# Performance work log

Measured on AMD Instinct MI355X. Metric: run time of the kernel, lower is better.

## Reference

```python
import jax, jax.numpy as jnp
import numpy as np

N = 10000
E = 160000
IN_C = 512
OUT_C = 1024
NEG_SLOPE = 0.2


def setup_inputs() -> dict:
    key = jax.random.key(0)
    ks = jax.random.split(key, 12)
    x = jax.random.normal(ks[0], (N, IN_C), dtype=jnp.float32)
    edge_index = jax.random.randint(ks[1], (2, E), 0, N, dtype=jnp.int32)
    s_in = 1.0 / np.sqrt(IN_C)
    s_out = 1.0 / np.sqrt(OUT_C)
    return {
        "x": x,
        "edge_index": edge_index,
        "W1": jax.random.normal(ks[2], (IN_C, OUT_C), dtype=jnp.float32) * s_in,
        "a_src1": jax.random.normal(ks[3], (OUT_C,), dtype=jnp.float32) * s_out,
        "a_dst1": jax.random.normal(ks[4], (OUT_C,), dtype=jnp.float32) * s_out,
        "b1": jnp.zeros((OUT_C,), dtype=jnp.float32),
        "W2": jax.random.normal(ks[5], (IN_C, OUT_C), dtype=jnp.float32) * s_in,
        "a_src2": jax.random.normal(ks[6], (OUT_C,), dtype=jnp.float32) * s_out,
        "a_dst2": jax.random.normal(ks[7], (OUT_C,), dtype=jnp.float32) * s_out,
        "b2": jnp.zeros((OUT_C,), dtype=jnp.float32),
        "prelu_a": jnp.asarray(0.25, dtype=jnp.float32),
        "Wp1": jax.random.normal(ks[8], (OUT_C, OUT_C), dtype=jnp.float32) * s_out,
        "bp1": jnp.zeros((OUT_C,), dtype=jnp.float32),
        "Wp2": jax.random.normal(ks[9], (OUT_C, 1024), dtype=jnp.float32) * s_out,
    }


def _gat_conv(x, src, dst, W, a_src, a_dst, b):
    # x: [N, in], W: [in, out]. PyG GATConv, heads=1, self-loops already in src/dst.
    h = x @ W  # [N, out]
    alpha_s = h @ a_src  # [N]
    alpha_d = h @ a_dst  # [N]
    e = alpha_s[src] + alpha_d[dst]  # [E+N]
    e = jnp.where(e >= 0, e, NEG_SLOPE * e)  # LeakyReLU(0.2)
    # segment softmax over destination nodes
    m = jax.ops.segment_max(e, dst, num_segments=N)  # [N]
    ex = jnp.exp(e - m[dst])
    denom = jax.ops.segment_sum(ex, dst, num_segments=N)  # [N], >=1 via self-loops
    alpha = ex / denom[dst]  # [E+N]
    out = jax.ops.segment_sum(alpha[:, None] * h[src], dst, num_segments=N)
    return out + b


def reference(x, edge_index, W1, a_src1, a_dst1, b1, W2, a_src2, a_dst2, b2,
              prelu_a, Wp1, bp1, Wp2):
    # add self loops (PyG GATConv default)
    loops = jnp.arange(N, dtype=edge_index.dtype)
    src = jnp.concatenate([edge_index[0], loops])
    dst = jnp.concatenate([edge_index[1], loops])

    def prelu(v):
        return jnp.where(v >= 0, v, prelu_a * v)

    h1 = prelu(_gat_conv(x, src, dst, W1, a_src1, a_dst1, b1))  # [N, 1024]
    h2 = prelu(_gat_conv(x, src, dst, W2, a_src2, a_dst2, b2))  # [N, 1024]
    h = h1 + h2

    # semantic attention: project -> mean over nodes -> softmax over 1024 dims
    w = jnp.tanh(h @ Wp1 + bp1) @ Wp2  # [N, 1024]
    w = w.mean(axis=0)  # [1024]
    att = jax.nn.softmax(w, axis=0)  # [1024] == beta.mean(0).squeeze()
    return att * h1 + (1.0 - att) * h2
```

## Files before the change

kernel.cpp:

```cpp
#include <hip/hip_runtime.h>

#define IN_C 512
#define OUT_C 1024
#define NC2 2048
#define NEG_SLOPE 0.2f

typedef short frag8 __attribute__((ext_vector_type(8)));
typedef float f32x4 __attribute__((ext_vector_type(4)));

#define GLOAD_LDS16(g, l) __builtin_amdgcn_global_load_lds(\
    (const __attribute__((address_space(1))) void*)(g), \
    (__attribute__((address_space(3))) void*)(l), 16, 0, 0)

__device__ __forceinline__ unsigned short f2b(float f){
  unsigned u = __float_as_uint(f);
  unsigned r = (u + 0x7fffu + ((u >> 16) & 1u)) >> 16;
  return (unsigned short)r;
}
__device__ __forceinline__ float leaky(float v){ return v >= 0.f ? v : NEG_SLOPE * v; }


__global__ void prep_kernel(const float* __restrict__ W1, const float* __restrict__ W2,
                            const float* __restrict__ Wp1,
                            const float* __restrict__ a_src1, const float* __restrict__ a_dst1,
                            const float* __restrict__ a_src2, const float* __restrict__ a_dst2,
                            unsigned short* __restrict__ WT, unsigned short* __restrict__ Wp1T,
                            float* __restrict__ uv){
  __shared__ float tile[32][33];
  int b = blockIdx.x;
  int tx = threadIdx.x & 31, ty = threadIdx.x >> 5;
  if (b < 1024){
    const float* in = (b >> 9) ? W2 : W1;
    int rowOff = (b >> 9) * OUT_C;
    int bb = b & 511;
    int c0 = (bb & 31) * 32, r0 = (bb >> 5) * 32;
    for (int i = ty; i < 32; i += 8)
      tile[i][tx] = in[(size_t)(r0 + i) * OUT_C + c0 + tx];
    __syncthreads();
    for (int i = ty; i < 32; i += 8)
      WT[(size_t)(c0 + i + rowOff) * IN_C + r0 + tx] = f2b(tile[tx][i]);
  } else if (b < 2048){
    int bb = b - 1024;
    int c0 = (bb & 31) * 32, r0 = (bb >> 5) * 32;
    for (int i = ty; i < 32; i += 8)
      tile[i][tx] = Wp1[(size_t)(r0 + i) * OUT_C + c0 + tx];
    __syncthreads();
    for (int i = ty; i < 32; i += 8)
      Wp1T[(size_t)(c0 + i) * OUT_C + r0 + tx] = f2b(tile[tx][i]);
  } else {
    int g = (b - 2048) * 4 + (threadIdx.x >> 6);
    int lane = threadIdx.x & 63;
    int which = g >> 9;
    int i = g & 511;
    const float* W = (which < 2) ? W1 : W2;
    const float* a = (which == 0) ? a_src1 : (which == 1) ? a_dst1 : (which == 2) ? a_src2 : a_dst2;
    const float* row = W + (size_t)i * OUT_C;
    float s = 0.f;
    for (int j = lane; j < OUT_C; j += 64) s += row[j] * a[j];
    for (int off = 32; off; off >>= 1) s += __shfl_down(s, off);
    if (lane == 0) uv[which * IN_C + i] = s;
  }
}


__global__ void alpha_kernel(const float* __restrict__ x, const float* __restrict__ uv,
                             unsigned short* __restrict__ xb,
                             float* __restrict__ as1, float* __restrict__ ad1,
                             float* __restrict__ as2, float* __restrict__ ad2,
                             float* __restrict__ self1, float* __restrict__ self2,
                             int* counts, int* cursor, float* colsum, float* wv){
  int n = blockIdx.x;
  int w = threadIdx.x >> 6, lane = threadIdx.x & 63;
  __shared__ float sh[4];
  if (threadIdx.x == 0){ counts[n] = 0; cursor[n] = 0; }
  if (n < 8){
    int i = n * 256 + threadIdx.x;
    if (i < 1024) colsum[i] = 0.f; else wv[i - 1024] = 0.f;
  }
  const float4* rv = (const float4*)(x + (size_t)n * IN_C);
  const float4* un = (const float4*)(uv + w * IN_C);
  float4 v0 = rv[lane], v1 = rv[lane + 64];
  float4 u0 = un[lane], u1 = un[lane + 64];
  float s = v0.x*u0.x + v0.y*u0.y + v0.z*u0.z + v0.w*u0.w
          + v1.x*u1.x + v1.y*u1.y + v1.z*u1.z + v1.w*u1.w;
  if (w == 0){
    ushort4 p0, p1;
    p0.x = f2b(v0.x); p0.y = f2b(v0.y); p0.z = f2b(v0.z); p0.w = f2b(v0.w);
    p1.x = f2b(v1.x); p1.y = f2b(v1.y); p1.z = f2b(v1.z); p1.w = f2b(v1.w);
    *(ushort4*)(xb + (size_t)n * IN_C + lane * 4) = p0;
    *(ushort4*)(xb + (size_t)n * IN_C + 256 + lane * 4) = p1;
  }
  for (int off = 32; off; off >>= 1) s += __shfl_down(s, off);
  if (lane == 0){
    sh[w] = s;
    if (w == 0) as1[n] = s;
    else if (w == 1) ad1[n] = s;
    else if (w == 2) as2[n] = s;
    else ad2[n] = s;
  }
  __syncthreads();
  if (threadIdx.x == 0){
    self1[n] = leaky(sh[0] + sh[1]);
    self2[n] = leaky(sh[2] + sh[3]);
  }
}


__global__ void histcount_kernel(const int* __restrict__ dst, int* counts, int E){
  int e = blockIdx.x * 256 + threadIdx.x;
  if (e < E) atomicAdd(&counts[dst[e]], 1);
}

__global__ void scanA_kernel(const int* __restrict__ counts, int* __restrict__ offs,
                             int* __restrict__ bsum, int n){
  __shared__ int wsum[4];
  int i = blockIdx.x * 256 + threadIdx.x;
  int wave = threadIdx.x >> 6, lane = threadIdx.x & 63;
  int v = (i < n) ? counts[i] : 0;
  int sc = v;
  for (int o = 1; o < 64; o <<= 1){
    int t = __shfl_up(sc, o);
    if (lane >= o) sc += t;
  }
  if (lane == 63) wsum[wave] = sc;
  __syncthreads();
  int wp = 0, tot = 0;
#pragma unroll
  for (int k = 0; k < 4; k++){
    int ws = wsum[k];
    if (k < wave) wp += ws;
    tot += ws;
  }
  if (i < n) offs[i] = wp + sc - v;
  if (threadIdx.x == 0) bsum[blockIdx.x] = tot;
}

__global__ void scanB_kernel(int* __restrict__ bsum, int nb){
  int lane = threadIdx.x;
  int v = (lane < nb) ? bsum[lane] : 0;
  int sc = v;
  for (int o = 1; o < 64; o <<= 1){
    int t = __shfl_up(sc, o);
    if (lane >= o) sc += t;
  }
  if (lane < nb) bsum[lane] = sc - v;
}

__global__ void scanC_kernel(int* __restrict__ offs, const int* __restrict__ bsum,
                             const float* __restrict__ self1, const float* __restrict__ self2,
                             float* __restrict__ den1, float* __restrict__ den2, int n){
  int i = blockIdx.x * 256 + threadIdx.x;
  if (i >= n) return;
  offs[i] += bsum[blockIdx.x];
  den1[i] = expf(self1[i]);
  den2[i] = expf(self2[i]);
}

__global__ void scatterexp_kernel(const int* __restrict__ src, const int* __restrict__ dst,
                                  const int* __restrict__ offs, int* cursor,
                                  const float* __restrict__ as1, const float* __restrict__ ad1,
                                  const float* __restrict__ as2, const float* __restrict__ ad2,
                                  int* __restrict__ nsrc, float* __restrict__ nw1, float* __restrict__ nw2,
                                  float* den1, float* den2, int E){
  int e = blockIdx.x * 256 + threadIdx.x;
  if (e >= E) return;
  int s = src[e], d = dst[e];
  int p = atomicAdd(&cursor[d], 1);
  int idx = offs[d] + p;
  float x1 = expf(leaky(as1[s] + ad1[d]));
  float x2 = expf(leaky(as2[s] + ad2[d]));
  nsrc[idx] = s; nw1[idx] = x1; nw2[idx] = x2;
  atomicAdd(&den1[d], x1);
  atomicAdd(&den2[d], x2);
}


#define AGG_FMA8(ACC, W, U) \
  ACC[0] += (W) * __uint_as_float(((unsigned)(U).x) << 16); \
  ACC[1] += (W) * __uint_as_float(((unsigned)(U).x) & 0xffff0000u); \
  ACC[2] += (W) * __uint_as_float(((unsigned)(U).y) << 16); \
  ACC[3] += (W) * __uint_as_float(((unsigned)(U).y) & 0xffff0000u); \
  ACC[4] += (W) * __uint_as_float(((unsigned)(U).z) << 16); \
  ACC[5] += (W) * __uint_as_float(((unsigned)(U).z) & 0xffff0000u); \
  ACC[6] += (W) * __uint_as_float(((unsigned)(U).w) << 16); \
  ACC[7] += (W) * __uint_as_float(((unsigned)(U).w) & 0xffff0000u);

__global__ __launch_bounds__(256) void aggx_kernel(
    const int* __restrict__ counts, const int* __restrict__ offs,
    const int* __restrict__ nsrc, const float* __restrict__ nw1, const float* __restrict__ nw2,
    const float* __restrict__ den1, const float* __restrict__ den2,
    const float* __restrict__ self1, const float* __restrict__ self2,
    const unsigned short* __restrict__ xb,
    unsigned short* __restrict__ xa1b, unsigned short* __restrict__ xa2b, int N){
  int wid = threadIdx.x >> 6, lane = threadIdx.x & 63;
  int d = blockIdx.x * 4 + wid;
  if (d >= N) return;
  float inv1 = 1.f / den1[d], inv2 = 1.f / den2[d];
  int deg = counts[d], off = offs[d];
  float acc1[8] = {0,0,0,0,0,0,0,0}, acc2[8] = {0,0,0,0,0,0,0,0};
  const unsigned short* Xb = xb + lane * 8;
  for (int base = 0; base < deg; base += 64){
    int i = base + lane;
    int s = 0; float w1 = 0.f, w2 = 0.f;
    if (i < deg){
      int p = off + i;
      s = nsrc[p];
      w1 = nw1[p] * inv1;
      w2 = nw2[p] * inv2;
    }
    int cnt = min(64, deg - base);
#pragma unroll 4
    for (int j = 0; j < cnt; j++){
      int sj = __shfl(s, j);
      float w1j = __shfl(w1, j);
      float w2j = __shfl(w2, j);
      int4 u = *(const int4*)(Xb + (size_t)sj * IN_C);
      AGG_FMA8(acc1, w1j, u)
      AGG_FMA8(acc2, w2j, u)
    }
  }
  {
    float ws1 = expf(self1[d]) * inv1;
    float ws2 = expf(self2[d]) * inv2;
    int4 u = *(const int4*)(Xb + (size_t)d * IN_C);
    AGG_FMA8(acc1, ws1, u)
    AGG_FMA8(acc2, ws2, u)
  }
  size_t outb = (size_t)d * IN_C + lane * 8;
  int4 o1, o2;
  o1.x = (int)((unsigned)f2b(acc1[0]) | ((unsigned)f2b(acc1[1]) << 16));
  o1.y = (int)((unsigned)f2b(acc1[2]) | ((unsigned)f2b(acc1[3]) << 16));
  o1.z = (int)((unsigned)f2b(acc1[4]) | ((unsigned)f2b(acc1[5]) << 16));
  o1.w = (int)((unsigned)f2b(acc1[6]) | ((unsigned)f2b(acc1[7]) << 16));
  o2.x = (int)((unsigned)f2b(acc2[0]) | ((unsigned)f2b(acc2[1]) << 16));
  o2.y = (int)((unsigned)f2b(acc2[2]) | ((unsigned)f2b(acc2[3]) << 16));
  o2.z = (int)((unsigned)f2b(acc2[4]) | ((unsigned)f2b(acc2[5]) << 16));
  o2.w = (int)((unsigned)f2b(acc2[6]) | ((unsigned)f2b(acc2[7]) << 16));
  *(int4*)(xa1b + outb) = o1;
  *(int4*)(xa2b + outb) = o2;
}


__global__ __launch_bounds__(256) void gemmh_kernel(const unsigned short* __restrict__ A1,
                                                    const unsigned short* __restrict__ A2,
                                                    const unsigned short* __restrict__ BT,
                                                    const float* __restrict__ b1,
                                                    const float* __restrict__ b2,
                                                    const float* __restrict__ prelu_a,
                                                    unsigned short* __restrict__ hsum,
                                                    unsigned short* __restrict__ hdiff,
                                                    int M, int Mtiles, int perx){
  const int bid = blockIdx.x;
  const int xcd = bid & 7;
  const int li = bid >> 3;
  const int bn_t = li & 7;
  const int bm_t = xcd * perx + (li >> 3);
  if (bm_t >= Mtiles) return;
  const int bm = bm_t * 64, bn = bn_t * 128;
  __shared__ unsigned short Al[64 * 32];
  __shared__ unsigned short Bl[128 * 32];
  const int t = threadIdx.x;
  const int lane = t & 63, wid = t >> 6;
  const int wj = wid;
  const int l16 = lane & 15, q = lane >> 4;
  const int lch = (lane & 3) * 8;
  f32x4 acc1[4][2] = {};
  f32x4 acc2[4][2] = {};
  const int arow = bm + wid * 16 + (lane >> 2);
  const int brow0 = bn + wid * 32 + (lane >> 2);
  const int ga = min(arow, M - 1);
  const unsigned short* pa1 = A1 + (size_t)ga * IN_C + lch;
  const unsigned short* pa2 = A2 + (size_t)ga * IN_C + lch;
  const unsigned short* pb0 = BT + (size_t)brow0 * IN_C + lch;
  const unsigned short* pb1 = BT + (size_t)(brow0 + 16) * IN_C + lch;
  const size_t boff2 = (size_t)OUT_C * IN_C;
  for (int k0 = 0; k0 < IN_C; k0 += 32){
    GLOAD_LDS16(pa1 + k0, &Al[(wid * 16) * 32]);
    GLOAD_LDS16(pb0 + k0, &Bl[(wid * 32) * 32]);
    GLOAD_LDS16(pb1 + k0, &Bl[(wid * 32 + 16) * 32]);
    __syncthreads();
    frag8 af[4], bf[2];
#pragma unroll
    for (int mi = 0; mi < 4; mi++) af[mi] = *(const frag8*)&Al[(mi*16 + l16) * 32 + q*8];
#pragma unroll
    for (int nj = 0; nj < 2; nj++) bf[nj] = *(const frag8*)&Bl[(wj*32 + nj*16 + l16) * 32 + q*8];
#pragma unroll
    for (int mi = 0; mi < 4; mi++)
#pragma unroll
      for (int nj = 0; nj < 2; nj++)
        acc1[mi][nj] = __builtin_amdgcn_mfma_f32_16x16x32_bf16(af[mi], bf[nj], acc1[mi][nj], 0, 0, 0);
    __syncthreads();
  }
  for (int k0 = 0; k0 < IN_C; k0 += 32){
    GLOAD_LDS16(pa2 + k0, &Al[(wid * 16) * 32]);
    GLOAD_LDS16(pb0 + boff2 + k0, &Bl[(wid * 32) * 32]);
    GLOAD_LDS16(pb1 + boff2 + k0, &Bl[(wid * 32 + 16) * 32]);
    __syncthreads();
    frag8 af[4], bf[2];
#pragma unroll
    for (int mi = 0; mi < 4; mi++) af[mi] = *(const frag8*)&Al[(mi*16 + l16) * 32 + q*8];
#pragma unroll
    for (int nj = 0; nj < 2; nj++) bf[nj] = *(const frag8*)&Bl[(wj*32 + nj*16 + l16) * 32 + q*8];
#pragma unroll
    for (int mi = 0; mi < 4; mi++)
#pragma unroll
      for (int nj = 0; nj < 2; nj++)
        acc2[mi][nj] = __builtin_amdgcn_mfma_f32_16x16x32_bf16(af[mi], bf[nj], acc2[mi][nj], 0, 0, 0);
    __syncthreads();
  }
  float pa = prelu_a[0];
#pragma unroll
  for (int mi = 0; mi < 4; mi++){
#pragma unroll
    for (int r = 0; r < 4; r++){
      int row = bm + mi*16 + q*4 + r;
      if (row >= M) continue;
#pragma unroll
      for (int nj = 0; nj < 2; nj++){
        int col = bn + wj*32 + nj*16 + l16;
        float v1 = acc1[mi][nj][r] + b1[col];
        v1 = v1 >= 0.f ? v1 : pa * v1;
        float v2 = acc2[mi][nj][r] + b2[col];
        v2 = v2 >= 0.f ? v2 : pa * v2;
        size_t idx = (size_t)row * OUT_C + col;
        hsum[idx]  = f2b(v1 + v2);
        hdiff[idx] = f2b(v1 - v2);
      }
    }
  }
}


__global__ __launch_bounds__(256) void gemm2_kernel(const unsigned short* __restrict__ A,
                                                    const unsigned short* __restrict__ BT,
                                                    const float* __restrict__ bp1,
                                                    float* __restrict__ colsum,
                                                    int M, int Mtiles, int perx){
  const int bid = blockIdx.x;
  const int xcd = bid & 7;
  const int li = bid >> 3;
  const int bn_t = li & 7;
  const int bm_t = xcd * perx + (li >> 3);
  if (bm_t >= Mtiles) return;
  const int bm = bm_t * 64, bn = bn_t * 128;
  __shared__ unsigned short Al[64 * 32];
  __shared__ unsigned short Bl[128 * 32];
  __shared__ float cs[128];
  const int t = threadIdx.x;
  const int lane = t & 63, wid = t >> 6;
  const int wj = wid;
  const int l16 = lane & 15, q = lane >> 4;
  const int lch = (lane & 3) * 8;
  if (t < 128) cs[t] = 0.f;
  f32x4 acc[4][2] = {};
  const int arow = bm + wid * 16 + (lane >> 2);
  const int brow0 = bn + wid * 32 + (lane >> 2);
  const int ga = min(arow, M - 1);
  const unsigned short* pa = A + (size_t)ga * OUT_C + lch;
  const unsigned short* pb0 = BT + (size_t)brow0 * OUT_C + lch;
  const unsigned short* pb1 = BT + (size_t)(brow0 + 16) * OUT_C + lch;
  for (int k0 = 0; k0 < OUT_C; k0 += 32){
    GLOAD_LDS16(pa + k0, &Al[(wid * 16) * 32]);
    GLOAD_LDS16(pb0 + k0, &Bl[(wid * 32) * 32]);
    GLOAD_LDS16(pb1 + k0, &Bl[(wid * 32 + 16) * 32]);
    __syncthreads();
    frag8 af[4], bf[2];
#pragma unroll
    for (int mi = 0; mi < 4; mi++) af[mi] = *(const frag8*)&Al[(mi*16 + l16) * 32 + q*8];
#pragma unroll
    for (int nj = 0; nj < 2; nj++) bf[nj] = *(const frag8*)&Bl[(wj*32 + nj*16 + l16) * 32 + q*8];
#pragma unroll
    for (int mi = 0; mi < 4; mi++)
#pragma unroll
      for (int nj = 0; nj < 2; nj++)
        acc[mi][nj] = __builtin_amdgcn_mfma_f32_16x16x32_bf16(af[mi], bf[nj], acc[mi][nj], 0, 0, 0);
    __syncthreads();
  }
#pragma unroll
  for (int nj = 0; nj < 2; nj++){
    int col = bn + wj*32 + nj*16 + l16;
    float bias = bp1[col];
    float p = 0.f;
#pragma unroll
    for (int mi = 0; mi < 4; mi++){
#pragma unroll
      for (int r = 0; r < 4; r++){
        int row = bm + mi*16 + q*4 + r;
        float tv = tanhf(acc[mi][nj][r] + bias);
        if (row < M) p += tv;
      }
    }
    p += __shfl_xor(p, 16);
    p += __shfl_xor(p, 32);
    if (q == 0) atomicAdd(&cs[wj*32 + nj*16 + l16], p);
  }
  __syncthreads();
  if (t < 128) atomicAdd(&colsum[bn + t], cs[t]);
}


__global__ void wproj_kernel(const float* __restrict__ colsum, const float* __restrict__ Wp2,
                             float* __restrict__ wv){
  int o = blockIdx.x * 256 + threadIdx.x;
  int c0 = blockIdx.y * 128;
  float acc = 0.f;
  for (int c = c0; c < c0 + 128; c++) acc += colsum[c] * Wp2[(size_t)c * OUT_C + o];
  atomicAdd(&wv[o], acc);
}

__global__ __launch_bounds__(1024) void softmax_kernel(const float* __restrict__ wv,
                                                       float* __restrict__ att, float invN){
  int o = threadIdx.x;
  __shared__ float red[1024];
  float w = wv[o] * invN;
  red[o] = w; __syncthreads();
  for (int s = 512; s > 0; s >>= 1){ if (o < s) red[o] = fmaxf(red[o], red[o + s]); __syncthreads(); }
  float m = red[0]; __syncthreads();
  float e = expf(w - m);
  red[o] = e; __syncthreads();
  for (int s = 512; s > 0; s >>= 1){ if (o < s) red[o] += red[o + s]; __syncthreads(); }
  att[o] = e / red[0];
}

__global__ void combine_kernel(const float* __restrict__ att, const unsigned short* __restrict__ hs,
                               const unsigned short* __restrict__ hd, float* __restrict__ out, int total8){
  int i = blockIdx.x * 256 + threadIdx.x;
  if (i >= total8) return;
  int colb = (i & 127) * 8;
  int4 us = ((const int4*)hs)[i];
  int4 ud = ((const int4*)hd)[i];
  float4 a0 = *(const float4*)(att + colb);
  float4 a1 = *(const float4*)(att + colb + 4);
  float o[8]; float sv, dv;
  sv = __uint_as_float(((unsigned)us.x) << 16);        dv = __uint_as_float(((unsigned)ud.x) << 16);
  o[0] = 0.5f * sv + (a0.x - 0.5f) * dv;
  sv = __uint_as_float(((unsigned)us.x) & 0xffff0000u); dv = __uint_as_float(((unsigned)ud.x) & 0xffff0000u);
  o[1] = 0.5f * sv + (a0.y - 0.5f) * dv;
  sv = __uint_as_float(((unsigned)us.y) << 16);        dv = __uint_as_float(((unsigned)ud.y) << 16);
  o[2] = 0.5f * sv + (a0.z - 0.5f) * dv;
  sv = __uint_as_float(((unsigned)us.y) & 0xffff0000u); dv = __uint_as_float(((unsigned)ud.y) & 0xffff0000u);
  o[3] = 0.5f * sv + (a0.w - 0.5f) * dv;
  sv = __uint_as_float(((unsigned)us.z) << 16);        dv = __uint_as_float(((unsigned)ud.z) << 16);
  o[4] = 0.5f * sv + (a1.x - 0.5f) * dv;
  sv = __uint_as_float(((unsigned)us.z) & 0xffff0000u); dv = __uint_as_float(((unsigned)ud.z) & 0xffff0000u);
  o[5] = 0.5f * sv + (a1.y - 0.5f) * dv;
  sv = __uint_as_float(((unsigned)us.w) << 16);        dv = __uint_as_float(((unsigned)ud.w) << 16);
  o[6] = 0.5f * sv + (a1.z - 0.5f) * dv;
  sv = __uint_as_float(((unsigned)us.w) & 0xffff0000u); dv = __uint_as_float(((unsigned)ud.w) & 0xffff0000u);
  o[7] = 0.5f * sv + (a1.w - 0.5f) * dv;
  float4 f0; f0.x = o[0]; f0.y = o[1]; f0.z = o[2]; f0.w = o[3];
  float4 f1; f1.x = o[4]; f1.y = o[5]; f1.z = o[6]; f1.w = o[7];
  *(float4*)(out + (size_t)i * 8) = f0;
  *(float4*)(out + (size_t)i * 8 + 4) = f1;
}


extern "C" void kernel_launch(void* const* d_in, const int* in_sizes, int n_in,
                              void* d_out, int out_size, void* d_ws, size_t ws_size,
                              hipStream_t stream){
  const float* x      = (const float*)d_in[0];
  const int*   edge   = (const int*)d_in[1];
  const float* W1     = (const float*)d_in[2];
  const float* a_src1 = (const float*)d_in[3];
  const float* a_dst1 = (const float*)d_in[4];
  const float* b1     = (const float*)d_in[5];
  const float* W2     = (const float*)d_in[6];
  const float* a_src2 = (const float*)d_in[7];
  const float* a_dst2 = (const float*)d_in[8];
  const float* b2     = (const float*)d_in[9];
  const float* prelu_a= (const float*)d_in[10];
  const float* Wp1    = (const float*)d_in[11];
  const float* bp1    = (const float*)d_in[12];
  const float* Wp2    = (const float*)d_in[13];
  const int N = in_sizes[0] / IN_C;
  const int E = in_sizes[1] / 2;
  const int* srcArr = edge;
  const int* dstArr = edge + E;

  char* ws = (char*)d_ws;
  size_t o = 0;
  auto alloc = [&](size_t b) -> char* {
    char* p = ws + o;
    o = (o + b + 255) & ~(size_t)255;
    return p;
  };
  unsigned short* xb    = (unsigned short*)alloc((size_t)N * IN_C * 2);
  unsigned short* WT    = (unsigned short*)alloc((size_t)NC2 * IN_C * 2);
  unsigned short* Wp1T  = (unsigned short*)alloc((size_t)OUT_C * OUT_C * 2);
  unsigned short* xa1b  = (unsigned short*)alloc((size_t)N * IN_C * 2);
  unsigned short* xa2b  = (unsigned short*)alloc((size_t)N * IN_C * 2);
  unsigned short* hsum  = (unsigned short*)alloc((size_t)N * OUT_C * 2);
  unsigned short* hdiff = (unsigned short*)alloc((size_t)N * OUT_C * 2);
  float*          uv    = (float*)alloc(4 * IN_C * 4);
  float*          as1   = (float*)alloc((size_t)4 * N * 4);
  float* ad1 = as1 + N; float* as2 = as1 + 2 * N; float* ad2 = as1 + 3 * N;
  float*          self1 = (float*)alloc((size_t)2 * N * 4); float* self2 = self1 + N;
  float*          den1  = (float*)alloc((size_t)2 * N * 4); float* den2 = den1 + N;
  int*            counts= (int*)alloc((size_t)N * 4);
  int*            offs  = (int*)alloc((size_t)(N + 1) * 4);
  int*            cursor= (int*)alloc((size_t)N * 4);
  int*            bsum  = (int*)alloc(64 * 4);
  int*            nsrc  = (int*)alloc((size_t)E * 4);
  float*          nw1   = (float*)alloc((size_t)E * 4);
  float*          nw2   = (float*)alloc((size_t)E * 4);
  float*          colsum= (float*)alloc(OUT_C * 4);
  float*          wv    = (float*)alloc(OUT_C * 4);
  float*          att   = (float*)alloc(OUT_C * 4);

  const int Mtiles = (N + 63) / 64;
  const int perx = (Mtiles + 7) / 8;
  const int gemmgrid = 8 * perx * 8;
  const int nchunk = (N + 255) / 256;

  prep_kernel<<<2560, 256, 0, stream>>>(W1, W2, Wp1, a_src1, a_dst1, a_src2, a_dst2, WT, Wp1T, uv);
  alpha_kernel<<<N, 256, 0, stream>>>(x, uv, xb, as1, ad1, as2, ad2, self1, self2,
                                      counts, cursor, colsum, wv);
  histcount_kernel<<<(E + 255) / 256, 256, 0, stream>>>(dstArr, counts, E);
  scanA_kernel<<<nchunk, 256, 0, stream>>>(counts, offs, bsum, N);
  scanB_kernel<<<1, 64, 0, stream>>>(bsum, nchunk);
  scanC_kernel<<<nchunk, 256, 0, stream>>>(offs, bsum, self1, self2, den1, den2, N);
  scatterexp_kernel<<<(E + 255) / 256, 256, 0, stream>>>(srcArr, dstArr, offs, cursor,
                                                         as1, ad1, as2, ad2,
                                                         nsrc, nw1, nw2, den1, den2, E);
  aggx_kernel<<<(N + 3) / 4, 256, 0, stream>>>(counts, offs, nsrc, nw1, nw2, den1, den2,
                                               self1, self2, xb, xa1b, xa2b, N);
  gemmh_kernel<<<gemmgrid, 256, 0, stream>>>(xa1b, xa2b, WT, b1, b2, prelu_a,
                                             hsum, hdiff, N, Mtiles, perx);
  gemm2_kernel<<<gemmgrid, 256, 0, stream>>>(hsum, Wp1T, bp1, colsum, N, Mtiles, perx);
  wproj_kernel<<<dim3(4, 8), 256, 0, stream>>>(colsum, Wp2, wv);
  softmax_kernel<<<1, 1024, 0, stream>>>(wv, att, 1.0f / (float)N);
  combine_kernel<<<(N * OUT_C / 8 + 255) / 256, 256, 0, stream>>>(att, hsum, hdiff, (float*)d_out,
                                                                  N * OUT_C / 8);
}
```

Before: 295.3 us.

## Fuse graph preprocessing kernels and compute softmax weights inside aggregation

```diff
diff --git a/kernel.cpp b/kernel.cpp
--- a/kernel.cpp
+++ b/kernel.cpp
@@ -25,7 +25,8 @@
                             const float* __restrict__ a_src1, const float* __restrict__ a_dst1,
                             const float* __restrict__ a_src2, const float* __restrict__ a_dst2,
                             unsigned short* __restrict__ WT, unsigned short* __restrict__ Wp1T,
-                            float* __restrict__ uv){
+                            float* __restrict__ uv, int* __restrict__ counts,
+                            int* __restrict__ cursor, int N){
   __shared__ float tile[32][33];
   int b = blockIdx.x;
   int tx = threadIdx.x & 31, ty = threadIdx.x >> 5;
@@ -47,7 +48,7 @@
     __syncthreads();
     for (int i = ty; i < 32; i += 8)
       Wp1T[(size_t)(c0 + i) * OUT_C + r0 + tx] = f2b(tile[tx][i]);
-  } else {
+  } else if (b < 2560){
     int g = (b - 2048) * 4 + (threadIdx.x >> 6);
     int lane = threadIdx.x & 63;
     int which = g >> 9;
@@ -59,20 +60,30 @@
     for (int j = lane; j < OUT_C; j += 64) s += row[j] * a[j];
     for (int off = 32; off; off >>= 1) s += __shfl_down(s, off);
     if (lane == 0) uv[which * IN_C + i] = s;
-  }
-}
-
-
-__global__ void alpha_kernel(const float* __restrict__ x, const float* __restrict__ uv,
-                             unsigned short* __restrict__ xb,
-                             float* __restrict__ as1, float* __restrict__ ad1,
-                             float* __restrict__ as2, float* __restrict__ ad2,
-                             float* __restrict__ self1, float* __restrict__ self2,
-                             int* counts, int* cursor, float* colsum, float* wv){
-  int n = blockIdx.x;
+  } else {
+    int i = (b - 2560) * 256 + threadIdx.x;
+    if (i < N){ counts[i] = 0; cursor[i] = 0; }
+  }
+}
+
+
+__global__ void alphahist_kernel(const float* __restrict__ x, const float* __restrict__ uv,
+                                 const int* __restrict__ dst,
+                                 unsigned short* __restrict__ xb,
+                                 float2* __restrict__ sa, float2* __restrict__ da,
+                                 float2* __restrict__ ese,
+                                 int* __restrict__ counts,
+                                 float* __restrict__ colsum, float* __restrict__ wv,
+                                 int N, int E){
+  int b = blockIdx.x;
+  if (b >= N){
+    int e = (b - N) * 256 + threadIdx.x;
+    if (e < E) atomicAdd(&counts[dst[e]], 1);
+    return;
+  }
+  int n = b;
   int w = threadIdx.x >> 6, lane = threadIdx.x & 63;
   __shared__ float sh[4];
-  if (threadIdx.x == 0){ counts[n] = 0; cursor[n] = 0; }
   if (n < 8){
     int i = n * 256 + threadIdx.x;
     if (i < 1024) colsum[i] = 0.f; else wv[i - 1024] = 0.f;
@@ -91,87 +102,56 @@
     *(ushort4*)(xb + (size_t)n * IN_C + 256 + lane * 4) = p1;
   }
   for (int off = 32; off; off >>= 1) s += __shfl_down(s, off);
-  if (lane == 0){
-    sh[w] = s;
-    if (w == 0) as1[n] = s;
-    else if (w == 1) ad1[n] = s;
-    else if (w == 2) as2[n] = s;
-    else ad2[n] = s;
-  }
+  if (lane == 0) sh[w] = s;
   __syncthreads();
   if (threadIdx.x == 0){
-    self1[n] = leaky(sh[0] + sh[1]);
-    self2[n] = leaky(sh[2] + sh[3]);
-  }
-}
-
-
-__global__ void histcount_kernel(const int* __restrict__ dst, int* counts, int E){
-  int e = blockIdx.x * 256 + threadIdx.x;
-  if (e < E) atomicAdd(&counts[dst[e]], 1);
-}
-
-__global__ void scanA_kernel(const int* __restrict__ counts, int* __restrict__ offs,
-                             int* __restrict__ bsum, int n){
-  __shared__ int wsum[4];
-  int i = blockIdx.x * 256 + threadIdx.x;
-  int wave = threadIdx.x >> 6, lane = threadIdx.x & 63;
-  int v = (i < n) ? counts[i] : 0;
-  int sc = v;
-  for (int o = 1; o < 64; o <<= 1){
-    int t = __shfl_up(sc, o);
-    if (lane >= o) sc += t;
-  }
-  if (lane == 63) wsum[wave] = sc;
+    float2 vsa; vsa.x = sh[0]; vsa.y = sh[2];
+    float2 vda; vda.x = sh[1]; vda.y = sh[3];
+    sa[n] = vsa; da[n] = vda;
+    float2 es;
+    es.x = expf(leaky(sh[0] + sh[1]));
+    es.y = expf(leaky(sh[2] + sh[3]));
+    ese[n] = es;
+  }
+}
+
+
+__global__ __launch_bounds__(1024) void scan_kernel(const int* __restrict__ counts,
+                                                    int* __restrict__ offs, int n){
+  __shared__ int ws[16];
+  __shared__ int base_s;
+  int tid = threadIdx.x, lane = tid & 63, wave = tid >> 6;
+  if (tid == 0) base_s = 0;
   __syncthreads();
-  int wp = 0, tot = 0;
-#pragma unroll
-  for (int k = 0; k < 4; k++){
-    int ws = wsum[k];
-    if (k < wave) wp += ws;
-    tot += ws;
-  }
-  if (i < n) offs[i] = wp + sc - v;
-  if (threadIdx.x == 0) bsum[blockIdx.x] = tot;
-}
-
-__global__ void scanB_kernel(int* __restrict__ bsum, int nb){
-  int lane = threadIdx.x;
-  int v = (lane < nb) ? bsum[lane] : 0;
-  int sc = v;
-  for (int o = 1; o < 64; o <<= 1){
-    int t = __shfl_up(sc, o);
-    if (lane >= o) sc += t;
-  }
-  if (lane < nb) bsum[lane] = sc - v;
-}
-
-__global__ void scanC_kernel(int* __restrict__ offs, const int* __restrict__ bsum,
-                             const float* __restrict__ self1, const float* __restrict__ self2,
-                             float* __restrict__ den1, float* __restrict__ den2, int n){
-  int i = blockIdx.x * 256 + threadIdx.x;
-  if (i >= n) return;
-  offs[i] += bsum[blockIdx.x];
-  den1[i] = expf(self1[i]);
-  den2[i] = expf(self2[i]);
-}
-
-__global__ void scatterexp_kernel(const int* __restrict__ src, const int* __restrict__ dst,
-                                  const int* __restrict__ offs, int* cursor,
-                                  const float* __restrict__ as1, const float* __restrict__ ad1,
-                                  const float* __restrict__ as2, const float* __restrict__ ad2,
-                                  int* __restrict__ nsrc, float* __restrict__ nw1, float* __restrict__ nw2,
-                                  float* den1, float* den2, int E){
+  for (int base = 0; base < n; base += 1024){
+    int i = base + tid;
+    int v = (i < n) ? counts[i] : 0;
+    int sc = v;
+    for (int o = 1; o < 64; o <<= 1){
+      int t = __shfl_up(sc, o);
+      if (lane >= o) sc += t;
+    }
+    if (lane == 63) ws[wave] = sc;
+    __syncthreads();
+    int wp = 0, tot = 0;
+#pragma unroll
+    for (int k = 0; k < 16; k++){ int w_ = ws[k]; if (k < wave) wp += w_; tot += w_; }
+    if (i < n) offs[i] = base_s + wp + sc - v;
+    __syncthreads();
+    if (tid == 0) base_s += tot;
+    __syncthreads();
+  }
+}
+
+
+__global__ void csr_kernel(const int* __restrict__ src, const int* __restrict__ dst,
+                           const int* __restrict__ offs, int* cursor,
+                           int* __restrict__ nsrc, int E){
   int e = blockIdx.x * 256 + threadIdx.x;
   if (e >= E) return;
-  int s = src[e], d = dst[e];
+  int d = dst[e];
   int p = atomicAdd(&cursor[d], 1);
-  int idx = offs[d] + p;
-  float x1 = expf(leaky(as1[s] + ad1[d]));
-  float x2 = expf(leaky(as2[s] + ad2[d]));
-  nsrc[idx] = s; nw1[idx] = x1; nw2[idx] = x2;
-  atomicAdd(&den1[d], x1);
-  atomicAdd(&den2[d], x2);
+  nsrc[offs[d] + p] = src[e];
 }
 
 
@@ -187,55 +167,62 @@
 
 __global__ __launch_bounds__(256) void aggx_kernel(
     const int* __restrict__ counts, const int* __restrict__ offs,
-    const int* __restrict__ nsrc, const float* __restrict__ nw1, const float* __restrict__ nw2,
-    const float* __restrict__ den1, const float* __restrict__ den2,
-    const float* __restrict__ self1, const float* __restrict__ self2,
+    const int* __restrict__ nsrc,
+    const float2* __restrict__ sa, const float2* __restrict__ da,
+    const float2* __restrict__ ese,
     const unsigned short* __restrict__ xb,
     unsigned short* __restrict__ xa1b, unsigned short* __restrict__ xa2b, int N){
   int wid = threadIdx.x >> 6, lane = threadIdx.x & 63;
   int d = blockIdx.x * 4 + wid;
   if (d >= N) return;
-  float inv1 = 1.f / den1[d], inv2 = 1.f / den2[d];
+  float2 dad = da[d];
   int deg = counts[d], off = offs[d];
   float acc1[8] = {0,0,0,0,0,0,0,0}, acc2[8] = {0,0,0,0,0,0,0,0};
+  float den1 = 0.f, den2 = 0.f;
   const unsigned short* Xb = xb + lane * 8;
   for (int base = 0; base < deg; base += 64){
     int i = base + lane;
-    int s = 0; float w1 = 0.f, w2 = 0.f;
+    int s = 0; float x1 = 0.f, x2 = 0.f;
     if (i < deg){
-      int p = off + i;
-      s = nsrc[p];
-      w1 = nw1[p] * inv1;
-      w2 = nw2[p] * inv2;
+      s = nsrc[off + i];
+      float2 sas = sa[s];
+      x1 = expf(leaky(sas.x + dad.x));
+      x2 = expf(leaky(sas.y + dad.y));
     }
+    den1 += x1; den2 += x2;
     int cnt = min(64, deg - base);
 #pragma unroll 4
     for (int j = 0; j < cnt; j++){
       int sj = __shfl(s, j);
-      float w1j = __shfl(w1, j);
-      float w2j = __shfl(w2, j);
+      float w1j = __shfl(x1, j);
+      float w2j = __shfl(x2, j);
       int4 u = *(const int4*)(Xb + (size_t)sj * IN_C);
       AGG_FMA8(acc1, w1j, u)
       AGG_FMA8(acc2, w2j, u)
     }
   }
+  for (int o = 32; o; o >>= 1){
+    den1 += __shfl_xor(den1, o);
+    den2 += __shfl_xor(den2, o);
+  }
+  float2 es = ese[d];
   {
-    float ws1 = expf(self1[d]) * inv1;
-    float ws2 = expf(self2[d]) * inv2;
     int4 u = *(const int4*)(Xb + (size_t)d * IN_C);
-    AGG_FMA8(acc1, ws1, u)
-    AGG_FMA8(acc2, ws2, u)
-  }
+    AGG_FMA8(acc1, es.x, u)
+    AGG_FMA8(acc2, es.y, u)
+  }
+  den1 += es.x; den2 += es.y;
+  float inv1 = 1.f / den1, inv2 = 1.f / den2;
   size_t outb = (size_t)d * IN_C + lane * 8;
   int4 o1, o2;
-  o1.x = (int)((unsigned)f2b(acc1[0]) | ((unsigned)f2b(acc1[1]) << 16));
-  o1.y = (int)((unsigned)f2b(acc1[2]) | ((unsigned)f2b(acc1[3]) << 16));
-  o1.z = (int)((unsigned)f2b(acc1[4]) | ((unsigned)f2b(acc1[5]) << 16));
-  o1.w = (int)((unsigned)f2b(acc1[6]) | ((unsigned)f2b(acc1[7]) << 16));
-  o2.x = (int)((unsigned)f2b(acc2[0]) | ((unsigned)f2b(acc2[1]) << 16));
-  o2.y = (int)((unsigned)f2b(acc2[2]) | ((unsigned)f2b(acc2[3]) << 16));
-  o2.z = (int)((unsigned)f2b(acc2[4]) | ((unsigned)f2b(acc2[5]) << 16));
-  o2.w = (int)((unsigned)f2b(acc2[6]) | ((unsigned)f2b(acc2[7]) << 16));
+  o1.x = (int)((unsigned)f2b(acc1[0]*inv1) | ((unsigned)f2b(acc1[1]*inv1) << 16));
+  o1.y = (int)((unsigned)f2b(acc1[2]*inv1) | ((unsigned)f2b(acc1[3]*inv1) << 16));
+  o1.z = (int)((unsigned)f2b(acc1[4]*inv1) | ((unsigned)f2b(acc1[5]*inv1) << 16));
+  o1.w = (int)((unsigned)f2b(acc1[6]*inv1) | ((unsigned)f2b(acc1[7]*inv1) << 16));
+  o2.x = (int)((unsigned)f2b(acc2[0]*inv2) | ((unsigned)f2b(acc2[1]*inv2) << 16));
+  o2.y = (int)((unsigned)f2b(acc2[2]*inv2) | ((unsigned)f2b(acc2[3]*inv2) << 16));
+  o2.z = (int)((unsigned)f2b(acc2[4]*inv2) | ((unsigned)f2b(acc2[5]*inv2) << 16));
+  o2.w = (int)((unsigned)f2b(acc2[6]*inv2) | ((unsigned)f2b(acc2[7]*inv2) << 16));
   *(int4*)(xa1b + outb) = o1;
   *(int4*)(xa2b + outb) = o2;
 }
@@ -492,17 +479,13 @@
   unsigned short* hsum  = (unsigned short*)alloc((size_t)N * OUT_C * 2);
   unsigned short* hdiff = (unsigned short*)alloc((size_t)N * OUT_C * 2);
   float*          uv    = (float*)alloc(4 * IN_C * 4);
-  float*          as1   = (float*)alloc((size_t)4 * N * 4);
-  float* ad1 = as1 + N; float* as2 = as1 + 2 * N; float* ad2 = as1 + 3 * N;
-  float*          self1 = (float*)alloc((size_t)2 * N * 4); float* self2 = self1 + N;
-  float*          den1  = (float*)alloc((size_t)2 * N * 4); float* den2 = den1 + N;
+  float2*         sa    = (float2*)alloc((size_t)N * 8);
+  float2*         da    = (float2*)alloc((size_t)N * 8);
+  float2*         ese   = (float2*)alloc((size_t)N * 8);
   int*            counts= (int*)alloc((size_t)N * 4);
   int*            offs  = (int*)alloc((size_t)(N + 1) * 4);
   int*            cursor= (int*)alloc((size_t)N * 4);
-  int*            bsum  = (int*)alloc(64 * 4);
   int*            nsrc  = (int*)alloc((size_t)E * 4);
-  float*          nw1   = (float*)alloc((size_t)E * 4);
-  float*          nw2   = (float*)alloc((size_t)E * 4);
   float*          colsum= (float*)alloc(OUT_C * 4);
   float*          wv    = (float*)alloc(OUT_C * 4);
   float*          att   = (float*)alloc(OUT_C * 4);
@@ -510,20 +493,17 @@
   const int Mtiles = (N + 63) / 64;
   const int perx = (Mtiles + 7) / 8;
   const int gemmgrid = 8 * perx * 8;
-  const int nchunk = (N + 255) / 256;
-
-  prep_kernel<<<2560, 256, 0, stream>>>(W1, W2, Wp1, a_src1, a_dst1, a_src2, a_dst2, WT, Wp1T, uv);
-  alpha_kernel<<<N, 256, 0, stream>>>(x, uv, xb, as1, ad1, as2, ad2, self1, self2,
-                                      counts, cursor, colsum, wv);
-  histcount_kernel<<<(E + 255) / 256, 256, 0, stream>>>(dstArr, counts, E);
-  scanA_kernel<<<nchunk, 256, 0, stream>>>(counts, offs, bsum, N);
-  scanB_kernel<<<1, 64, 0, stream>>>(bsum, nchunk);
-  scanC_kernel<<<nchunk, 256, 0, stream>>>(offs, bsum, self1, self2, den1, den2, N);
-  scatterexp_kernel<<<(E + 255) / 256, 256, 0, stream>>>(srcArr, dstArr, offs, cursor,
-                                                         as1, ad1, as2, ad2,
-                                                         nsrc, nw1, nw2, den1, den2, E);
-  aggx_kernel<<<(N + 3) / 4, 256, 0, stream>>>(counts, offs, nsrc, nw1, nw2, den1, den2,
-                                               self1, self2, xb, xa1b, xa2b, N);
+  const int zblocks = (N + 255) / 256;
+  const int eblocks = (E + 255) / 256;
+
+  prep_kernel<<<2560 + zblocks, 256, 0, stream>>>(W1, W2, Wp1, a_src1, a_dst1, a_src2, a_dst2,
+                                                  WT, Wp1T, uv, counts, cursor, N);
+  alphahist_kernel<<<N + eblocks, 256, 0, stream>>>(x, uv, dstArr, xb, sa, da, ese,
+                                                    counts, colsum, wv, N, E);
+  scan_kernel<<<1, 1024, 0, stream>>>(counts, offs, N);
+  csr_kernel<<<eblocks, 256, 0, stream>>>(srcArr, dstArr, offs, cursor, nsrc, E);
+  aggx_kernel<<<(N + 3) / 4, 256, 0, stream>>>(counts, offs, nsrc, sa, da, ese,
+                                               xb, xa1b, xa2b, N);
   gemmh_kernel<<<gemmgrid, 256, 0, stream>>>(xa1b, xa2b, WT, b1, b2, prelu_a,
                                              hsum, hdiff, N, Mtiles, perx);
   gemm2_kernel<<<gemmgrid, 256, 0, stream>>>(hsum, Wp1T, bp1, colsum, N, Mtiles, perx);
```

New measurement: 279.9 us. 1.05x faster.
